# Performance work log

Hardware: AMD Instinct MI355X
Metric: run time of the kernel (lower is better)

## Reference

```python
import jax, jax.numpy as jnp
import numpy as np

B, S, D, H, DH, F = 1, 2048, 1024, 16, 64, 4096
LN_EPS = 1e-5

def _layernorm(x, w, b):
    mu = jnp.mean(x, axis=-1, keepdims=True)
    xc = x - mu
    var = jnp.mean(xc * xc, axis=-1, keepdims=True)
    return xc * jax.lax.rsqrt(var + LN_EPS) * w + b

def setup_inputs() -> dict:
    key = jax.random.key(0)
    ks = jax.random.split(key, 8)
    sc = lambda fan: 1.0 / np.sqrt(fan)
    return {
        'resid_pre': jax.random.normal(ks[0], (B, S, D), jnp.float32),
        'ln1_w': jnp.ones((D,), jnp.float32), 'ln1_b': jnp.zeros((D,), jnp.float32),
        'W_Q': jax.random.normal(ks[1], (H, D, DH), jnp.float32) * sc(D),
        'b_Q': jnp.zeros((H, DH), jnp.float32),
        'W_K': jax.random.normal(ks[2], (H, D, DH), jnp.float32) * sc(D),
        'b_K': jnp.zeros((H, DH), jnp.float32),
        'W_V': jax.random.normal(ks[3], (H, D, DH), jnp.float32) * sc(D),
        'b_V': jnp.zeros((H, DH), jnp.float32),
        'W_O': jax.random.normal(ks[4], (H, DH, D), jnp.float32) * sc(DH),
        'b_O': jnp.zeros((D,), jnp.float32),
        'mask_logits': jax.random.normal(ks[5], (H,), jnp.float32) * 0.01 + 1.0,
        'ln2_w': jnp.ones((D,), jnp.float32), 'ln2_b': jnp.zeros((D,), jnp.float32),
        'W_in': jax.random.normal(ks[6], (D, F), jnp.float32) * sc(D),
        'b_in': jnp.zeros((F,), jnp.float32),
        'W_out': jax.random.normal(ks[7], (F, D), jnp.float32) * sc(F),
        'b_out': jnp.zeros((D,), jnp.float32),
    }

def reference(resid_pre, ln1_w, ln1_b, W_Q, b_Q, W_K, b_K, W_V, b_V, W_O, b_O,
              mask_logits, ln2_w, ln2_b, W_in, b_in, W_out, b_out):
    x = _layernorm(resid_pre, ln1_w, ln1_b)                          # [B,S,D]
    q = jnp.einsum('bsd,hdk->bshk', x, W_Q) + b_Q                    # [B,S,H,DH]
    k = jnp.einsum('bsd,hdk->bshk', x, W_K) + b_K
    v = jnp.einsum('bsd,hdk->bshk', x, W_V) + b_V
    scores = jnp.einsum('bqhk,bshk->bhqs', q, k) / jnp.sqrt(jnp.asarray(DH, q.dtype))
    causal = jnp.tril(jnp.ones((S, S), bool))                        # [S,S]
    scores = jnp.where(causal, scores, -jnp.inf)
    pattern = jax.nn.softmax(scores, axis=-1)
    pattern = jnp.where(jnp.isnan(pattern), jnp.zeros_like(pattern), pattern)
    z = jnp.einsum('bhqs,bshk->bqhk', pattern, v)                    # [B,S,H,DH]
    # deterministic gumbel-sigmoid mask: per-head hard gate
    head_mask = (mask_logits > 0.0).astype(z.dtype)                  # [H]
    masked_z = z * head_mask[None, None, :, None]
    attn_out = jnp.einsum('bqhk,hkd->bqd', masked_z, W_O) + b_O      # [B,S,D]
    resid_mid = resid_pre + attn_out
    m = _layernorm(resid_mid, ln2_w, ln2_b)
    mlp_out = jax.nn.gelu(m @ W_in + b_in) @ W_out + b_out
    return resid_mid + mlp_out
```

## Files before the change

kernel.cpp:

```cpp
#include <hip/hip_runtime.h>
#include <math.h>

typedef unsigned short u16;
typedef __attribute__((ext_vector_type(8))) short bf16x8;
typedef __attribute__((ext_vector_type(4))) float f32x4;

#define S_LEN 2048
#define D_MODEL 1024
#define N_HEADS 16
#define D_HEAD 64
#define F_MLP 4096
#define N_QKV 3072
#define QK_LD 2048
#define NSPLIT 4

__device__ __forceinline__ u16 f2b(float f) {
    union { float f; unsigned u; } x; x.f = f;
    unsigned r = x.u + 0x7fffu + ((x.u >> 16) & 1u);
    return (u16)(r >> 16);
}
__device__ __forceinline__ float b2f(u16 v) {
    union { unsigned u; float f; } x; x.u = ((unsigned)v) << 16; return x.f;
}

__device__ __forceinline__ void gload_lds16(const u16* g, u16* l) {
    __builtin_amdgcn_global_load_lds((const __attribute__((address_space(1))) unsigned int*)g,
                                     (__attribute__((address_space(3))) unsigned int*)l, 16, 0, 0);
}

__global__ __launch_bounds__(256) void prep_kernel(
        const float* __restrict__ W_Q, const float* __restrict__ W_K, const float* __restrict__ W_V,
        const float* __restrict__ W_O, const float* __restrict__ W_in, const float* __restrict__ W_out,
        u16* __restrict__ WT_qkv, u16* __restrict__ WT_O, u16* __restrict__ WT_in, u16* __restrict__ WT_out,
        const float* __restrict__ bq, const float* __restrict__ bk, const float* __restrict__ bv,
        float* __restrict__ qkvb,
        const float* __restrict__ resid_pre, const float* __restrict__ ln1_w,
        const float* __restrict__ ln1_b, u16* __restrict__ xln) {
    const int bid = blockIdx.x;
    const int tid = threadIdx.x;

    if (bid < 12288) {
        __shared__ float t[32][33];
        const float* src; u16* dst; int C, out_ld, bx, by;
        if (bid < 3072) {
            const int which = bid >> 10, r = bid & 1023;
            const int bz = r >> 6;
            by = (r >> 1) & 31; bx = r & 1;
            src = (which == 0 ? W_Q : which == 1 ? W_K : W_V) + (long)bz * 65536;
            dst = WT_qkv + ((size_t)which * 1024 + bz * 64) * 1024;
            C = 64; out_ld = 1024;
        } else if (bid < 4096) {
            const int r = bid - 3072;
            bx = r & 31; by = r >> 5;
            src = W_O; dst = WT_O; C = 1024; out_ld = 1024;
        } else if (bid < 8192) {
            const int r = bid - 4096;
            bx = r & 127; by = r >> 7;
            src = W_in; dst = WT_in; C = 4096; out_ld = 1024;
        } else {
            const int r = bid - 8192;
            bx = r & 31; by = r >> 5;
            src = W_out; dst = WT_out; C = 1024; out_ld = 4096;
        }
        const int c0 = bx * 32, r0 = by * 32;
        const int tx = tid & 31, ty = tid >> 5;
        #pragma unroll
        for (int i = 0; i < 32; i += 8)
            t[ty + i][tx] = src[(long)(r0 + ty + i) * C + c0 + tx];
        __syncthreads();
        #pragma unroll
        for (int i = 0; i < 32; i += 8)
            dst[(long)(c0 + ty + i) * out_ld + r0 + tx] = f2b(t[tx][ty + i]);
    } else if (bid < 14336) {
        const int row = bid - 12288;
        const float4* xr = (const float4*)(resid_pre + (long)row * D_MODEL);
        float4 v = xr[tid];
        float s = v.x + v.y + v.z + v.w;
        float ss = v.x * v.x + v.y * v.y + v.z * v.z + v.w * v.w;
        #pragma unroll
        for (int o = 1; o < 64; o <<= 1) { s += __shfl_xor(s, o, 64); ss += __shfl_xor(ss, o, 64); }
        __shared__ float sh[8];
        const int wave = tid >> 6, lane = tid & 63;
        if (lane == 0) { sh[wave] = s; sh[4 + wave] = ss; }
        __syncthreads();
        s = sh[0] + sh[1] + sh[2] + sh[3];
        ss = sh[4] + sh[5] + sh[6] + sh[7];
        const float mu = s * (1.0f / D_MODEL);
        const float var = ss * (1.0f / D_MODEL) - mu * mu;
        const float rstd = rsqrtf(var + 1e-5f);
        float4 wv = ((const float4*)ln1_w)[tid];
        float4 bv = ((const float4*)ln1_b)[tid];
        u16 o4[4];
        o4[0] = f2b((v.x - mu) * rstd * wv.x + bv.x);
        o4[1] = f2b((v.y - mu) * rstd * wv.y + bv.y);
        o4[2] = f2b((v.z - mu) * rstd * wv.z + bv.z);
        o4[3] = f2b((v.w - mu) * rstd * wv.w + bv.w);
        *(ushort4*)(xln + (long)row * D_MODEL + tid * 4) = *(ushort4*)o4;
    } else {
        const int i = (bid - 14336) * 256 + tid;
        float v = (i < 1024) ? bq[i] : (i < 2048) ? bk[i - 1024] : bv[i - 2048];
        qkvb[i] = v;
    }
}

__global__ __launch_bounds__(256) void reduce_split4(const u16* __restrict__ p,
                                                     const float* __restrict__ bias,
                                                     const float* __restrict__ addend,
                                                     float* __restrict__ out) {
    const size_t i = (size_t)blockIdx.x * 256 + threadIdx.x;
    const size_t MN4 = (size_t)S_LEN * D_MODEL / 4;
    float ox = 0.f, oy = 0.f, oz = 0.f, ow = 0.f;
    #pragma unroll
    for (int s = 0; s < NSPLIT; ++s) {
        ushort4 v = ((const ushort4*)p)[(size_t)s * MN4 + i];
        ox += b2f(v.x); oy += b2f(v.y); oz += b2f(v.z); ow += b2f(v.w);
    }
    float4 b4 = ((const float4*)bias)[i & (D_MODEL / 4 - 1)];
    float4 a4 = ((const float4*)addend)[i];
    float4 o;
    o.x = ox + b4.x + a4.x; o.y = oy + b4.y + a4.y;
    o.z = oz + b4.z + a4.z; o.w = ow + b4.w + a4.w;
    ((float4*)out)[i] = o;
}

__global__ __launch_bounds__(256) void reduce4_ln(const u16* __restrict__ p,
                                                  const float* __restrict__ bias,
                                                  const float* __restrict__ addend,
                                                  const float* __restrict__ lnw,
                                                  const float* __restrict__ lnb,
                                                  float* __restrict__ rmid,
                                                  u16* __restrict__ out) {
    const int row = blockIdx.x, tid = threadIdx.x;
    const size_t MN4 = (size_t)S_LEN * D_MODEL / 4;
    const size_t i = (size_t)row * (D_MODEL / 4) + tid;
    float ox = 0.f, oy = 0.f, oz = 0.f, ow = 0.f;
    #pragma unroll
    for (int sp = 0; sp < NSPLIT; ++sp) {
        ushort4 v = ((const ushort4*)p)[(size_t)sp * MN4 + i];
        ox += b2f(v.x); oy += b2f(v.y); oz += b2f(v.z); ow += b2f(v.w);
    }
    float4 b4 = ((const float4*)bias)[tid];
    float4 a4 = ((const float4*)addend)[i];
    float4 o;
    o.x = ox + b4.x + a4.x; o.y = oy + b4.y + a4.y;
    o.z = oz + b4.z + a4.z; o.w = ow + b4.w + a4.w;
    ((float4*)rmid)[i] = o;

    float s = o.x + o.y + o.z + o.w;
    float ss = o.x * o.x + o.y * o.y + o.z * o.z + o.w * o.w;
    #pragma unroll
    for (int of = 1; of < 64; of <<= 1) { s += __shfl_xor(s, of, 64); ss += __shfl_xor(ss, of, 64); }
    __shared__ float sh[8];
    const int wave = tid >> 6, lane = tid & 63;
    if (lane == 0) { sh[wave] = s; sh[4 + wave] = ss; }
    __syncthreads();
    s = sh[0] + sh[1] + sh[2] + sh[3];
    ss = sh[4] + sh[5] + sh[6] + sh[7];
    const float mu = s * (1.0f / D_MODEL);
    const float var = ss * (1.0f / D_MODEL) - mu * mu;
    const float rstd = rsqrtf(var + 1e-5f);
    float4 wv = ((const float4*)lnw)[tid];
    float4 bv = ((const float4*)lnb)[tid];
    u16 o4[4];
    o4[0] = f2b((o.x - mu) * rstd * wv.x + bv.x);
    o4[1] = f2b((o.y - mu) * rstd * wv.y + bv.y);
    o4[2] = f2b((o.z - mu) * rstd * wv.z + bv.z);
    o4[3] = f2b((o.w - mu) * rstd * wv.w + bv.w);
    *(ushort4*)(out + (long)row * D_MODEL + tid * 4) = *(ushort4*)o4;
}

__global__ __launch_bounds__(256) void gemm_qkv(const u16* __restrict__ A,
                                                const u16* __restrict__ BT,
                                                const float* __restrict__ bias,
                                                u16* __restrict__ Cout,
                                                u16* __restrict__ vt,
                                                int K, int gx) {
    __shared__ u16 SMEM[24576];
    u16* As = SMEM;
    u16* Bs = SMEM + 8192;

    const int lin = blockIdx.x;
    const int q = gridDim.x >> 3;
    const int swz = (lin & 7) * q + (lin >> 3);
    const int bx = swz % gx;
    const int by = swz / gx;

    const int bm = by * 64, bn = bx * 128;
    const int tid = threadIdx.x;
    const int wave = tid >> 6, lane = tid & 63;
    const int wm = (wave & 1) * 32, wn = (wave >> 1) * 64;
    const int l16 = lane & 15, lq = lane >> 4;

    f32x4 acc[2][4] = {};

    auto stage = [&](int buf, int kk) {
        #pragma unroll
        for (int c = 0; c < 2; ++c) {
            const int idx = c * 256 + tid;
            const int row = idx >> 3;
            const int cbu = ((idx & 7) ^ (row & 7)) << 3;
            gload_lds16(A + (size_t)(bm + row) * K + kk + cbu,
                        &As[buf * 4096 + (c * 256 + wave * 64) * 8]);
        }
        #pragma unroll
        for (int c = 0; c < 4; ++c) {
            const int idx = c * 256 + tid;
            const int row = idx >> 3;
            const int cbu = ((idx & 7) ^ (row & 7)) << 3;
            gload_lds16(BT + (size_t)(bn + row) * K + kk + cbu,
                        &Bs[buf * 8192 + (c * 256 + wave * 64) * 8]);
        }
    };

    const int nk = K >> 6;
    stage(0, 0);
    __syncthreads();

    int buf = 0;
    for (int t = 0; t < nk; ++t) {
        if (t + 1 < nk) stage(buf ^ 1, (t + 1) * 64);
        #pragma unroll
        for (int kc = 0; kc < 2; ++kc) {
            bf16x8 af[2], bf[4];
            #pragma unroll
            for (int i = 0; i < 2; ++i) {
                const int rA = wm + i * 16 + l16;
                af[i] = *(const bf16x8*)&As[buf * 4096 + rA * 64 + ((kc * 32 + lq * 8) ^ ((rA & 7) << 3))];
            }
            #pragma unroll
            for (int j = 0; j < 4; ++j) {
                const int rB = wn + j * 16 + l16;
                bf[j] = *(const bf16x8*)&Bs[buf * 8192 + rB * 64 + ((kc * 32 + lq * 8) ^ ((rB & 7) << 3))];
            }
            #pragma unroll
            for (int i = 0; i < 2; ++i)
                #pragma unroll
                for (int j = 0; j < 4; ++j)
                    acc[i][j] = __builtin_amdgcn_mfma_f32_16x16x32_bf16(af[i], bf[j], acc[i][j], 0, 0, 0);
        }
        __syncthreads();
        buf ^= 1;
    }

    if (bn < 2048) {
        #pragma unroll
        for (int i = 0; i < 2; ++i) {
            const int row = bm + wm + i * 16 + lq * 4;
            #pragma unroll
            for (int j = 0; j < 4; ++j) {
                const int col = bn + wn + j * 16 + l16;
                const float bcol = bias[col];
                const float sc = (col < 1024) ? 0.125f : 1.0f;
                #pragma unroll
                for (int r = 0; r < 4; ++r)
                    Cout[(size_t)(row + r) * QK_LD + col] = f2b((acc[i][j][r] + bcol) * sc);
            }
        }
    } else {
        u16* Ct = SMEM;
        #pragma unroll
        for (int i = 0; i < 2; ++i) {
            const int rl = wm + i * 16 + lq * 4;
            #pragma unroll
            for (int j = 0; j < 4; ++j) {
                const int c = wn + j * 16 + l16;
                const float bcol = bias[bn + c];
                #pragma unroll
                for (int r = 0; r < 4; ++r)
                    Ct[c * 72 + rl + r] = f2b(acc[i][j][r] + bcol);
            }
        }
        __syncthreads();
        #pragma unroll
        for (int g = 0; g < 4; ++g) {
            const int idx = g * 256 + tid;
            const int c = idx >> 3, j = idx & 7;
            bf16x8 v = *(const bf16x8*)&Ct[c * 72 + j * 8];
            *(bf16x8*)(vt + (size_t)(bn - 2048 + c) * S_LEN + bm + j * 8) = v;
        }
    }
}

template <int MODE>
__global__ __launch_bounds__(256) void gemm128(const u16* __restrict__ A,
                                               const u16* __restrict__ BT,
                                               const float* __restrict__ bias,
                                               void* __restrict__ Cout,
                                               int M, int N, int K, int kb,
                                               int gx, int gy) {
    __shared__ u16 SMEM[2][16384];

    const int lin = blockIdx.x;
    const int q = gridDim.x >> 3;
    const int swz = (lin & 7) * q + (lin >> 3);
    const int bx = swz % gx;
    const int rest = swz / gx;
    const int by = rest % gy;
    const int bz = rest / gy;

    const int bm = by * 128, bn = bx * 128;
    const int k0base = bz * kb;
    const int tid = threadIdx.x;
    const int wave = tid >> 6, lane = tid & 63;
    const int wm = (wave >> 1) * 64, wn = (wave & 1) * 64;
    const int l16 = lane & 15, lq = lane >> 4;

    f32x4 acc[4][4] = {};

    auto stage = [&](int buf, int kk) {
        #pragma unroll
        for (int c = 0; c < 4; ++c) {
            const int idx = c * 256 + tid;
            const int row = idx >> 3;
            const int cbu = ((idx & 7) ^ (row & 7)) << 3;
            gload_lds16(A  + (size_t)(bm + row) * K + kk + cbu, &SMEM[buf][(c * 256 + wave * 64) * 8]);
            gload_lds16(BT + (size_t)(bn + row) * K + kk + cbu, &SMEM[buf][8192 + (c * 256 + wave * 64) * 8]);
        }
    };

    const int nk = kb >> 6;
    stage(0, k0base);
    __syncthreads();

    int buf = 0;
    for (int t = 0; t < nk; ++t) {
        if (t + 1 < nk) stage(buf ^ 1, k0base + (t + 1) * 64);
        #pragma unroll
        for (int kc = 0; kc < 2; ++kc) {
            bf16x8 af[4], bf[4];
            #pragma unroll
            for (int i = 0; i < 4; ++i) {
                const int rA = wm + i * 16 + l16;
                af[i] = *(const bf16x8*)&SMEM[buf][rA * 64 + ((kc * 32 + lq * 8) ^ ((rA & 7) << 3))];
                const int rB = wn + i * 16 + l16;
                bf[i] = *(const bf16x8*)&SMEM[buf][8192 + rB * 64 + ((kc * 32 + lq * 8) ^ ((rB & 7) << 3))];
            }
            #pragma unroll
            for (int i = 0; i < 4; ++i)
                #pragma unroll
                for (int j = 0; j < 4; ++j)
                    acc[i][j] = __builtin_amdgcn_mfma_f32_16x16x32_bf16(af[i], bf[j], acc[i][j], 0, 0, 0);
        }
        __syncthreads();
        buf ^= 1;
    }

    #pragma unroll
    for (int i = 0; i < 4; ++i) {
        const int row = bm + wm + i * 16 + lq * 4;
        #pragma unroll
        for (int j = 0; j < 4; ++j) {
            const int col = bn + wn + j * 16 + l16;
            if (MODE == 1) {
                u16* out = (u16*)Cout + (size_t)bz * M * N;
                #pragma unroll
                for (int r = 0; r < 4; ++r)
                    out[(size_t)(row + r) * N + col] = f2b(acc[i][j][r]);
            } else {
                const float bcol = bias[col];
                #pragma unroll
                for (int r = 0; r < 4; ++r) {
                    float v = acc[i][j][r] + bcol;
                    float g_ = 0.5f * v * (1.0f + tanhf(0.7978845608028654f * (v + 0.044715f * v * v * v)));
                    ((u16*)Cout)[(size_t)(row + r) * N + col] = f2b(g_);
                }
            }
        }
    }
}

__global__ __launch_bounds__(256) void attn_split(const u16* __restrict__ qk,
                                                  const u16* __restrict__ vT,
                                                  u16* __restrict__ accP,
                                                  float* __restrict__ lP) {
    const int tid = threadIdx.x;
    const int wave = tid >> 6, lane = tid & 63;
    const int l16 = lane & 15, lq = lane >> 4;
    const int b = blockIdx.x;
    const int p1 = (b ^ (b >> 8)) & 1;
    const int h = (b >> 1) & 15;
    const int qh = (b >> 5) & 15;
    const int sp = (b >> 9) & 3;
    const int qquad = p1 ? (31 - qh) : qh;
    const int qi = qquad * 4 + wave;
    const int qb = qi * 16;
    const int nt = qquad + 1;
    const int base = nt >> 2, rem = nt & 3;
    const int t0 = sp * base + (sp < rem ? sp : rem);
    const int t1 = t0 + base + (sp < rem ? 1 : 0);
    const int QC = h * 64, KC = 1024 + h * 64;
    const u16* vh = vT + (size_t)(h * 64) * S_LEN;

    __shared__ u16 KVs[2][2][64 * 64];
    __shared__ u16 Pb[4][16][64];

    const bf16x8 ones = {0x3F80, 0x3F80, 0x3F80, 0x3F80, 0x3F80, 0x3F80, 0x3F80, 0x3F80};

    bf16x8 qf[2];
    #pragma unroll
    for (int kc = 0; kc < 2; ++kc)
        qf[kc] = *(const bf16x8*)(qk + (size_t)(qb + l16) * QK_LD + QC + kc * 32 + lq * 8);

    f32x4 acc[4] = {};
    f32x4 accl = {};

    auto stageKV = [&](int buf, int t) {
        const int sk0 = t << 6;
        #pragma unroll
        for (int c = 0; c < 2; ++c) {
            const int idx = c * 256 + tid;
            const int row = idx >> 3;
            const int cbu = ((idx & 7) ^ (row & 7)) << 3;
            u16* ldst = &KVs[buf][0][(size_t)(c * 256 + wave * 64) * 8];
            gload_lds16(qk + (size_t)(sk0 + row) * QK_LD + KC + cbu, ldst);
            u16* ldstV = &KVs[buf][1][(size_t)(c * 256 + wave * 64) * 8];
            gload_lds16(vh + (size_t)row * S_LEN + sk0 + cbu, ldstV);
        }
    };

    if (t0 < t1) { stageKV(0, t0); __syncthreads(); }
    int buf = 0;
    for (int t = t0; t < t1; ++t) {
        if (t + 1 < t1) stageKV(buf ^ 1, t + 1);

        f32x4 s[4];
        #pragma unroll
        for (int nf = 0; nf < 4; ++nf) {
            const int rK = nf * 16 + l16;
            f32x4 a = {};
            #pragma unroll
            for (int kc = 0; kc < 2; ++kc) {
                bf16x8 kf = *(const bf16x8*)&KVs[buf][0][rK * 64 + ((kc * 32 + lq * 8) ^ ((rK & 7) << 3))];
                a = __builtin_amdgcn_mfma_f32_16x16x32_bf16(qf[kc], kf, a, 0, 0, 0);
            }
            s[nf] = a;
        }

        bf16x8 vf[8];
        #pragma unroll
        for (int d = 0; d < 4; ++d) {
            const int rV = d * 16 + l16;
            vf[d * 2]     = *(const bf16x8*)&KVs[buf][1][rV * 64 + ((lq * 8) ^ ((rV & 7) << 3))];
            vf[d * 2 + 1] = *(const bf16x8*)&KVs[buf][1][rV * 64 + ((32 + lq * 8) ^ ((rV & 7) << 3))];
        }

        if (t == nt - 1) {
            const int sk0 = t << 6;
            #pragma unroll
            for (int nf = 0; nf < 4; ++nf) {
                const int sk = sk0 + nf * 16 + l16;
                #pragma unroll
                for (int r = 0; r < 4; ++r) {
                    const int qrow = qb + lq * 4 + r;
                    s[nf][r] = (sk <= qrow) ? s[nf][r] : -3.0e38f;
                }
            }
        }

        #pragma unroll
        for (int nf = 0; nf < 4; ++nf)
            #pragma unroll
            for (int r = 0; r < 4; ++r) {
                const float p = __expf(s[nf][r]);
                const int row = lq * 4 + r, col = nf * 16 + l16;
                Pb[wave][row][col ^ ((row & 7) << 3)] = (u16)(__float_as_uint(p) >> 16);
            }

        bf16x8 pf0 = *(const bf16x8*)&Pb[wave][l16][(lq * 8) ^ ((l16 & 7) << 3)];
        bf16x8 pf1 = *(const bf16x8*)&Pb[wave][l16][(32 + lq * 8) ^ ((l16 & 7) << 3)];

        accl = __builtin_amdgcn_mfma_f32_16x16x32_bf16(pf0, ones, accl, 0, 0, 0);
        accl = __builtin_amdgcn_mfma_f32_16x16x32_bf16(pf1, ones, accl, 0, 0, 0);

        #pragma unroll
        for (int d = 0; d < 4; ++d) {
            acc[d] = __builtin_amdgcn_mfma_f32_16x16x32_bf16(pf0, vf[d * 2],     acc[d], 0, 0, 0);
            acc[d] = __builtin_amdgcn_mfma_f32_16x16x32_bf16(pf1, vf[d * 2 + 1], acc[d], 0, 0, 0);
        }

        __syncthreads();
        buf ^= 1;
    }

    const size_t pb = ((size_t)(sp * N_HEADS + h) * S_LEN + qb);
    #pragma unroll
    for (int r = 0; r < 4; ++r) {
        const size_t row = pb + lq * 4 + r;
        #pragma unroll
        for (int d = 0; d < 4; ++d)
            accP[row * 64 + d * 16 + l16] = f2b(acc[d][r]);
        if (l16 == 0)
            lP[row] = accl[r];
    }
}

__global__ __launch_bounds__(256) void attn_merge(const u16* __restrict__ accP,
                                                  const float* __restrict__ lP,
                                                  const float* __restrict__ mask_logits,
                                                  u16* __restrict__ z) {
    const int tid = threadIdx.x;
    const int lane = tid & 63;
    const int rt = blockIdx.x * 4 + (tid >> 6);
    const int h = rt >> 11, row = rt & 2047;

    float l = 0.0f, o = 0.0f;
    #pragma unroll
    for (int s = 0; s < NSPLIT; ++s) {
        const size_t base = (size_t)(s * N_HEADS + h) * S_LEN + row;
        l += lP[base];
        o += b2f(accP[base * 64 + lane]);
    }
    const float gate = (mask_logits[h] > 0.0f) ? 1.0f : 0.0f;
    z[(size_t)row * D_MODEL + h * 64 + lane] = f2b(gate * o / l);
}

extern "C" void kernel_launch(void* const* d_in, const int* in_sizes, int n_in,
                              void* d_out, int out_size, void* d_ws, size_t ws_size,
                              hipStream_t stream) {
    const float* resid_pre  = (const float*)d_in[0];
    const float* ln1_w      = (const float*)d_in[1];
    const float* ln1_b      = (const float*)d_in[2];
    const float* W_Q        = (const float*)d_in[3];
    const float* b_Q        = (const float*)d_in[4];
    const float* W_K        = (const float*)d_in[5];
    const float* b_K        = (const float*)d_in[6];
    const float* W_V        = (const float*)d_in[7];
    const float* b_V        = (const float*)d_in[8];
    const float* W_O        = (const float*)d_in[9];
    const float* b_O        = (const float*)d_in[10];
    const float* mask_logits= (const float*)d_in[11];
    const float* ln2_w      = (const float*)d_in[12];
    const float* ln2_b      = (const float*)d_in[13];
    const float* W_in       = (const float*)d_in[14];
    const float* b_in       = (const float*)d_in[15];
    const float* W_out      = (const float*)d_in[16];
    const float* b_out      = (const float*)d_in[17];

    char* p = (char*)d_ws;
    u16* WT_qkv = (u16*)p; p += (size_t)N_QKV * D_MODEL * 2;
    u16* WT_O   = (u16*)p; p += (size_t)D_MODEL * D_MODEL * 2;
    u16* WT_in  = (u16*)p; p += (size_t)F_MLP * D_MODEL * 2;
    u16* WT_out = (u16*)p; p += (size_t)D_MODEL * F_MLP * 2;
    float* qkvb = (float*)p; p += (size_t)N_QKV * 4;
    u16* xln    = (u16*)p; p += (size_t)S_LEN * D_MODEL * 2;
    u16* qk     = (u16*)p; p += (size_t)S_LEN * QK_LD * 2;
    u16* vTb    = (u16*)p; p += (size_t)D_MODEL * S_LEN * 2;
    u16* zb     = (u16*)p; p += (size_t)S_LEN * D_MODEL * 2;
    float* rmid = (float*)p; p += (size_t)S_LEN * D_MODEL * 4;
    u16* mb     = (u16*)p; p += (size_t)S_LEN * D_MODEL * 2;
    u16* hb     = (u16*)p; p += (size_t)S_LEN * F_MLP * 2;
    u16* pbuf   = (u16*)p; p += (size_t)NSPLIT * S_LEN * D_MODEL * 2;

    u16* accP = (u16*)hb;
    float* lP = (float*)(accP + (size_t)NSPLIT * N_HEADS * S_LEN * 64);

    prep_kernel<<<dim3(14348), 256, 0, stream>>>(W_Q, W_K, W_V, W_O, W_in, W_out,
                                                 WT_qkv, WT_O, WT_in, WT_out,
                                                 b_Q, b_K, b_V, qkvb,
                                                 resid_pre, ln1_w, ln1_b, xln);

    gemm_qkv<<<dim3(768), 256, 0, stream>>>(xln, WT_qkv, qkvb, qk, vTb, D_MODEL, 24);

    attn_split<<<dim3(2048), 256, 0, stream>>>(qk, vTb, accP, lP);
    attn_merge<<<dim3(8192), 256, 0, stream>>>(accP, lP, mask_logits, zb);

    gemm128<1><<<dim3(512), 256, 0, stream>>>(zb, WT_O, nullptr, pbuf,
                                              S_LEN, D_MODEL, D_MODEL, 256, 8, 16);
    reduce4_ln<<<S_LEN, 256, 0, stream>>>(pbuf, b_O, resid_pre, ln2_w, ln2_b, rmid, mb);

    gemm128<2><<<dim3(512), 256, 0, stream>>>(mb, WT_in, b_in, hb,
                                              S_LEN, F_MLP, D_MODEL, D_MODEL, 32, 16);

    gemm128<1><<<dim3(512), 256, 0, stream>>>(hb, WT_out, nullptr, pbuf,
                                              S_LEN, D_MODEL, F_MLP, 1024, 8, 16);
    reduce_split4<<<2048, 256, 0, stream>>>(pbuf, b_out, rmid, (float*)d_out);
}
```

Baseline: 138.0 us.

## Process 32 query rows per wave in split attention to reuse staged K/V

Each wave in the split-K attention kernel now handles two 16-row query subtiles (a 128-row block per workgroup instead of 64), so every staged K/V tile in LDS feeds twice as many MFMAs and the grid halves. Causal skipping is tracked per subtile so the lower subtile skips tiles past its diagonal. The Q scale now folds in log2(e), letting the softmax use exp2f instead of __expf. The cost is more registers per wave, fewer workgroups, and some divergence on the last diagonal tiles.

```diff
diff --git a/kernel.cpp b/kernel.cpp
--- a/kernel.cpp
+++ b/kernel.cpp
@@ -250,7 +250,7 @@
             for (int j = 0; j < 4; ++j) {
                 const int col = bn + wn + j * 16 + l16;
                 const float bcol = bias[col];
-                const float sc = (col < 1024) ? 0.125f : 1.0f;
+                const float sc = (col < 1024) ? 0.18033688011112042f : 1.0f;
                 #pragma unroll
                 for (int r = 0; r < 4; ++r)
                     Cout[(size_t)(row + r) * QK_LD + col] = f2b((acc[i][j][r] + bcol) * sc);
@@ -379,30 +379,33 @@
     const int b = blockIdx.x;
     const int p1 = (b ^ (b >> 8)) & 1;
     const int h = (b >> 1) & 15;
-    const int qh = (b >> 5) & 15;
-    const int sp = (b >> 9) & 3;
-    const int qquad = p1 ? (31 - qh) : qh;
-    const int qi = qquad * 4 + wave;
-    const int qb = qi * 16;
-    const int nt = qquad + 1;
-    const int base = nt >> 2, rem = nt & 3;
+    const int qoh = (b >> 5) & 7;
+    const int sp = (b >> 8) & 3;
+    const int po = p1 ? (15 - qoh) : qoh;
+    const int qb = po * 128 + wave * 32;
+    const int nt_blk = 2 * po + 2;
+    const int base = nt_blk >> 2, rem = nt_blk & 3;
     const int t0 = sp * base + (sp < rem ? sp : rem);
     const int t1 = t0 + base + (sp < rem ? 1 : 0);
+    const int dt0 = qb >> 6, dt1 = (qb + 16) >> 6;
+    const int ntw0 = dt0 + 1, ntw1 = dt1 + 1;
     const int QC = h * 64, KC = 1024 + h * 64;
     const u16* vh = vT + (size_t)(h * 64) * S_LEN;
 
     __shared__ u16 KVs[2][2][64 * 64];
-    __shared__ u16 Pb[4][16][64];
+    __shared__ u16 Pb[4][2][16][64];
 
     const bf16x8 ones = {0x3F80, 0x3F80, 0x3F80, 0x3F80, 0x3F80, 0x3F80, 0x3F80, 0x3F80};
 
-    bf16x8 qf[2];
+    bf16x8 qf0[2], qf1[2];
     #pragma unroll
-    for (int kc = 0; kc < 2; ++kc)
-        qf[kc] = *(const bf16x8*)(qk + (size_t)(qb + l16) * QK_LD + QC + kc * 32 + lq * 8);
-
-    f32x4 acc[4] = {};
-    f32x4 accl = {};
+    for (int kc = 0; kc < 2; ++kc) {
+        qf0[kc] = *(const bf16x8*)(qk + (size_t)(qb + l16) * QK_LD + QC + kc * 32 + lq * 8);
+        qf1[kc] = *(const bf16x8*)(qk + (size_t)(qb + 16 + l16) * QK_LD + QC + kc * 32 + lq * 8);
+    }
+
+    f32x4 acc0[4] = {}, acc1[4] = {};
+    f32x4 accl0 = {}, accl1 = {};
 
     auto stageKV = [&](int buf, int t) {
         const int sk0 = t << 6;
@@ -423,74 +426,95 @@
     for (int t = t0; t < t1; ++t) {
         if (t + 1 < t1) stageKV(buf ^ 1, t + 1);
 
-        f32x4 s[4];
-        #pragma unroll
-        for (int nf = 0; nf < 4; ++nf) {
-            const int rK = nf * 16 + l16;
-            f32x4 a = {};
-            #pragma unroll
-            for (int kc = 0; kc < 2; ++kc) {
-                bf16x8 kf = *(const bf16x8*)&KVs[buf][0][rK * 64 + ((kc * 32 + lq * 8) ^ ((rK & 7) << 3))];
-                a = __builtin_amdgcn_mfma_f32_16x16x32_bf16(qf[kc], kf, a, 0, 0, 0);
-            }
-            s[nf] = a;
-        }
-
-        bf16x8 vf[8];
-        #pragma unroll
-        for (int d = 0; d < 4; ++d) {
-            const int rV = d * 16 + l16;
-            vf[d * 2]     = *(const bf16x8*)&KVs[buf][1][rV * 64 + ((lq * 8) ^ ((rV & 7) << 3))];
-            vf[d * 2 + 1] = *(const bf16x8*)&KVs[buf][1][rV * 64 + ((32 + lq * 8) ^ ((rV & 7) << 3))];
-        }
-
-        if (t == nt - 1) {
+        if (t < ntw1) {
             const int sk0 = t << 6;
+
+            f32x4 s0[4], s1[4];
             #pragma unroll
             for (int nf = 0; nf < 4; ++nf) {
-                const int sk = sk0 + nf * 16 + l16;
-                #pragma unroll
-                for (int r = 0; r < 4; ++r) {
-                    const int qrow = qb + lq * 4 + r;
-                    s[nf][r] = (sk <= qrow) ? s[nf][r] : -3.0e38f;
+                const int rK = nf * 16 + l16;
+                bf16x8 kf0 = *(const bf16x8*)&KVs[buf][0][rK * 64 + ((lq * 8) ^ ((rK & 7) << 3))];
+                bf16x8 kf1 = *(const bf16x8*)&KVs[buf][0][rK * 64 + ((32 + lq * 8) ^ ((rK & 7) << 3))];
+                f32x4 a1 = {};
+                a1 = __builtin_amdgcn_mfma_f32_16x16x32_bf16(qf1[0], kf0, a1, 0, 0, 0);
+                a1 = __builtin_amdgcn_mfma_f32_16x16x32_bf16(qf1[1], kf1, a1, 0, 0, 0);
+                s1[nf] = a1;
+                if (t < ntw0) {
+                    f32x4 a0 = {};
+                    a0 = __builtin_amdgcn_mfma_f32_16x16x32_bf16(qf0[0], kf0, a0, 0, 0, 0);
+                    a0 = __builtin_amdgcn_mfma_f32_16x16x32_bf16(qf0[1], kf1, a0, 0, 0, 0);
+                    s0[nf] = a0;
                 }
             }
-        }
-
-        #pragma unroll
-        for (int nf = 0; nf < 4; ++nf)
-            #pragma unroll
-            for (int r = 0; r < 4; ++r) {
-                const float p = __expf(s[nf][r]);
-                const int row = lq * 4 + r, col = nf * 16 + l16;
-                Pb[wave][row][col ^ ((row & 7) << 3)] = (u16)(__float_as_uint(p) >> 16);
-            }
-
-        bf16x8 pf0 = *(const bf16x8*)&Pb[wave][l16][(lq * 8) ^ ((l16 & 7) << 3)];
-        bf16x8 pf1 = *(const bf16x8*)&Pb[wave][l16][(32 + lq * 8) ^ ((l16 & 7) << 3)];
-
-        accl = __builtin_amdgcn_mfma_f32_16x16x32_bf16(pf0, ones, accl, 0, 0, 0);
-        accl = __builtin_amdgcn_mfma_f32_16x16x32_bf16(pf1, ones, accl, 0, 0, 0);
-
-        #pragma unroll
-        for (int d = 0; d < 4; ++d) {
-            acc[d] = __builtin_amdgcn_mfma_f32_16x16x32_bf16(pf0, vf[d * 2],     acc[d], 0, 0, 0);
-            acc[d] = __builtin_amdgcn_mfma_f32_16x16x32_bf16(pf1, vf[d * 2 + 1], acc[d], 0, 0, 0);
+
+            bf16x8 vf[8];
+            #pragma unroll
+            for (int d = 0; d < 4; ++d) {
+                const int rV = d * 16 + l16;
+                vf[d * 2]     = *(const bf16x8*)&KVs[buf][1][rV * 64 + ((lq * 8) ^ ((rV & 7) << 3))];
+                vf[d * 2 + 1] = *(const bf16x8*)&KVs[buf][1][rV * 64 + ((32 + lq * 8) ^ ((rV & 7) << 3))];
+            }
+
+            if (t == dt1) {
+                #pragma unroll
+                for (int nf = 0; nf < 4; ++nf) {
+                    const int sk = sk0 + nf * 16 + l16;
+                    #pragma unroll
+                    for (int r = 0; r < 4; ++r)
+                        s1[nf][r] = (sk <= qb + 16 + lq * 4 + r) ? s1[nf][r] : -3.0e38f;
+                }
+            }
+            if (t < ntw0 && t == dt0) {
+                #pragma unroll
+                for (int nf = 0; nf < 4; ++nf) {
+                    const int sk = sk0 + nf * 16 + l16;
+                    #pragma unroll
+                    for (int r = 0; r < 4; ++r)
+                        s0[nf][r] = (sk <= qb + lq * 4 + r) ? s0[nf][r] : -3.0e38f;
+                }
+            }
+
+            auto SUB = [&](f32x4* s, f32x4* acc, f32x4& accl, int sub) {
+                #pragma unroll
+                for (int nf = 0; nf < 4; ++nf)
+                    #pragma unroll
+                    for (int r = 0; r < 4; ++r) {
+                        const float pv = exp2f(s[nf][r]);
+                        const int row = lq * 4 + r, col = nf * 16 + l16;
+                        Pb[wave][sub][row][col ^ ((row & 7) << 3)] = (u16)(__float_as_uint(pv) >> 16);
+                    }
+                bf16x8 pf0 = *(const bf16x8*)&Pb[wave][sub][l16][(lq * 8) ^ ((l16 & 7) << 3)];
+                bf16x8 pf1 = *(const bf16x8*)&Pb[wave][sub][l16][(32 + lq * 8) ^ ((l16 & 7) << 3)];
+                accl = __builtin_amdgcn_mfma_f32_16x16x32_bf16(pf0, ones, accl, 0, 0, 0);
+                accl = __builtin_amdgcn_mfma_f32_16x16x32_bf16(pf1, ones, accl, 0, 0, 0);
+                #pragma unroll
+                for (int d = 0; d < 4; ++d) {
+                    acc[d] = __builtin_amdgcn_mfma_f32_16x16x32_bf16(pf0, vf[d * 2],     acc[d], 0, 0, 0);
+                    acc[d] = __builtin_amdgcn_mfma_f32_16x16x32_bf16(pf1, vf[d * 2 + 1], acc[d], 0, 0, 0);
+                }
+            };
+            SUB(s1, acc1, accl1, 1);
+            if (t < ntw0) SUB(s0, acc0, accl0, 0);
         }
 
         __syncthreads();
         buf ^= 1;
     }
 
-    const size_t pb = ((size_t)(sp * N_HEADS + h) * S_LEN + qb);
+    const size_t pbase = ((size_t)(sp * N_HEADS + h) * S_LEN + qb);
     #pragma unroll
     for (int r = 0; r < 4; ++r) {
-        const size_t row = pb + lq * 4 + r;
-        #pragma unroll
-        for (int d = 0; d < 4; ++d)
-            accP[row * 64 + d * 16 + l16] = f2b(acc[d][r]);
-        if (l16 == 0)
-            lP[row] = accl[r];
+        const size_t row0 = pbase + lq * 4 + r;
+        const size_t row1 = pbase + 16 + lq * 4 + r;
+        #pragma unroll
+        for (int d = 0; d < 4; ++d) {
+            accP[row0 * 64 + d * 16 + l16] = f2b(acc0[d][r]);
+            accP[row1 * 64 + d * 16 + l16] = f2b(acc1[d][r]);
+        }
+        if (l16 == 0) {
+            lP[row0] = accl0[r];
+            lP[row1] = accl1[r];
+        }
     }
 }
 
@@ -561,7 +585,7 @@
 
     gemm_qkv<<<dim3(768), 256, 0, stream>>>(xln, WT_qkv, qkvb, qk, vTb, D_MODEL, 24);
 
-    attn_split<<<dim3(2048), 256, 0, stream>>>(qk, vTb, accP, lP);
+    attn_split<<<dim3(1024), 256, 0, stream>>>(qk, vTb, accP, lP);
     attn_merge<<<dim3(8192), 256, 0, stream>>>(accP, lP, mask_logits, zb);
 
     gemm128<1><<<dim3(512), 256, 0, stream>>>(zb, WT_O, nullptr, pbuf,
```

After: 141.6 us. 1.03x slower.
